# Optimization experiments

Hardware: AMD Instinct MI355X
Metric: run time of the kernel (lower is better)

## Reference

```python
import jax, jax.numpy as jnp
import numpy as np
from jax import lax

WIN = 9  # NCC window per axis (default [9]*3)

# 3x3x3 edge/shape kernels, shape [O=1, I=1, 3, 3, 3]
_LAP = np.zeros((3, 3, 3), np.float32)
_LAP[1, 1, 1] = 6.0
_LAP[0, 1, 1] = _LAP[2, 1, 1] = -1.0
_LAP[1, 0, 1] = _LAP[1, 2, 1] = -1.0
_LAP[1, 1, 0] = _LAP[1, 1, 2] = -1.0
LAP_K = jnp.asarray(_LAP)[None, None]

_row = np.array([[-1.0, 0.0, 1.0], [-2.0, 0.0, 2.0], [-1.0, 0.0, 1.0]], np.float32)
SOBEL_X = jnp.asarray(np.stack([_row, _row, _row], axis=0))[None, None]
_plane = np.array([[-1.0, -2.0, -1.0], [-1.0, -2.0, -1.0], [-1.0, -2.0, -1.0]], np.float32)
SOBEL_Y = jnp.asarray(np.stack([_plane, np.zeros((3, 3), np.float32), -_plane], axis=0))[None, None]
_zp = np.array([[-1.0, -1.0, -1.0], [0.0, 0.0, 0.0], [1.0, 1.0, 1.0]], np.float32)
SOBEL_Z = jnp.asarray(np.stack([_zp, 2.0 * _zp, _zp], axis=0))[None, None]


def conv3d(x, k, pad):
    # x: [N,C,D,H,W], k: [O,I,kd,kh,kw]
    return lax.conv_general_dilated(x, k, (1, 1, 1), [(pad, pad)] * 3)


def box_sum(x, win=WIN):
    # Separable all-ones box filter == dense ones conv (same math, fewer FLOPs)
    pad = win // 2
    for axis in range(3):
        kshape = [1, 1, 1, 1, 1]
        kshape[2 + axis] = win
        k = jnp.ones(kshape, x.dtype)
        padding = [(pad, pad) if a == axis else (0, 0) for a in range(3)]
        x = lax.conv_general_dilated(x, k, (1, 1, 1), padding)
    return x


def ncc_vxm(Ii, Ji, win=WIN):
    win_size = float(win ** 3)
    I2, J2, IJ = Ii * Ii, Ji * Ji, Ii * Ji
    I_sum = box_sum(Ii, win)
    J_sum = box_sum(Ji, win)
    I2_sum = box_sum(I2, win)
    J2_sum = box_sum(J2, win)
    IJ_sum = box_sum(IJ, win)
    u_I = I_sum / win_size
    u_J = J_sum / win_size
    cross = IJ_sum - u_J * I_sum - u_I * J_sum + u_I * u_J * win_size
    I_var = I2_sum - 2.0 * u_I * I_sum + u_I * u_I * win_size
    J_var = J2_sum - 2.0 * u_J * J_sum + u_J * u_J * win_size
    cc = cross * cross / (I_var * J_var + 1e-5)
    return -jnp.mean(cc)


def edge_detection(v):
    return conv3d(v, LAP_K, pad=1)


def shape_detection(v):
    gx = conv3d(v, SOBEL_X, pad=1)
    gy = conv3d(v, SOBEL_Y, pad=1)
    gz = conv3d(v, SOBEL_Z, pad=1)
    return jnp.sqrt(gx * gx + gy * gy + gz * gz)


def setup_inputs() -> dict:
    key = jax.random.key(0)
    k1, k2 = jax.random.split(key)
    shape = (1, 1, 160, 192, 160)
    y_true = jax.random.uniform(k1, shape, dtype=jnp.float32)
    y_pred = jax.random.uniform(k2, shape, dtype=jnp.float32)
    return {"y_true": y_true, "y_pred": y_pred}


def reference(y_true, y_pred):
    loss_orig = ncc_vxm(y_true, y_pred)
    loss_edge = ncc_vxm(edge_detection(y_true), edge_detection(y_pred))
    loss_shape = ncc_vxm(shape_detection(y_true), shape_detection(y_pred))
    return 0.8 * loss_orig + 0.1 * loss_edge + 0.1 * loss_shape
```

## Files before the change

### kernel.cpp

```cpp
#include <hip/hip_runtime.h>
#include <hip/hip_fp16.h>
#include <math.h>

#define DD 160
#define HHH 192
#define WWW 160
constexpr int HW = HHH * WWW;
constexpr int NV = DD * HHH * WWW;
constexpr int W4 = WWW / 4;
constexpr int HC = 4;
constexpr int DC = 4;
constexpr int SC = 8;
constexpr int SCF = 4;

constexpr int NB_WH  = (W4 * DD * (HHH / HC)) / 256;
constexpr int NB_SO  = (W4 * HHH * (DD / SC)) / 256;
constexpr int NB_LAP = (NV / 4) / 256;
constexpr int NB_DCC = (W4 * HHH * (DD / DC)) / 256;
constexpr int NB_FU  = (W4 * HHH * (DD / SCF)) / 256;

__device__ __forceinline__ int xcd_swz(int b, int n) {
    int q = n >> 3;
    return (b & 7) * q + (b >> 3);
}

__device__ __forceinline__ float4 ldg4(const float* __restrict__ p, int idx, bool ok) {
    float4 z = make_float4(0.f, 0.f, 0.f, 0.f);
    return ok ? *(const float4*)(p + idx) : z;
}

__device__ __forceinline__ void st_h4(__half* __restrict__ t, int idx,
                                      float s0, float s1, float s2, float s3) {
    union { __half2 h2[2]; uint2 u; } pk;
    pk.h2[0] = __floats2half2_rn(s0, s1);
    pk.h2[1] = __floats2half2_rn(s2, s3);
    *(uint2*)(t + idx) = pk.u;
}

__device__ __forceinline__ void ld_h4(const __half* __restrict__ t, int idx, float o[4]) {
    union { __half2 h2[2]; uint2 u; } pk;
    pk.u = *(const uint2*)(t + idx);
    o[0] = __low2float(pk.h2[0]); o[1] = __high2float(pk.h2[0]);
    o[2] = __low2float(pk.h2[1]); o[3] = __high2float(pk.h2[1]);
}

__device__ void fused_body(int t, const float* __restrict__ p,
                           __half* __restrict__ olap, __half* __restrict__ osob) {
    int w = (t % W4) * 4;
    int h = (t / W4) % HHH;
    int c = t / (W4 * HHH);
    int d0 = c * SCF;

    float A1[3][4], A2[3][4], A3[3][4];
    float P6[6], PP4[4], PH[4];
#pragma unroll
    for (int j = 0; j < 3; j++)
#pragma unroll
        for (int k = 0; k < 4; k++) { A1[j][k] = 0.f; A2[j][k] = 0.f; A3[j][k] = 0.f; }
#pragma unroll
    for (int k = 0; k < 6; k++) P6[k] = 0.f;
#pragma unroll
    for (int k = 0; k < 4; k++) { PP4[k] = 0.f; PH[k] = 0.f; }

#pragma unroll
    for (int i = 0; i < SCF + 2; i++) {
        int s = d0 - 1 + i;
#pragma unroll
        for (int k = 0; k < 4; k++) {
            A1[0][k] = A1[1][k]; A2[0][k] = A2[1][k]; A3[0][k] = A3[1][k];
            A1[1][k] = A1[2][k]; A2[1][k] = A2[2][k]; A3[1][k] = A3[2][k];
        }
        float C6[6] = {0.f, 0.f, 0.f, 0.f, 0.f, 0.f};
        float CH[4] = {0.f, 0.f, 0.f, 0.f};
#pragma unroll
        for (int k = 0; k < 4; k++) { A1[2][k] = 0.f; A2[2][k] = 0.f; A3[2][k] = 0.f; }
        if (s >= 0 && s < DD) {
#pragma unroll
            for (int kh = -1; kh <= 1; kh++) {
                int h2 = h + kh;
                if ((unsigned)h2 < (unsigned)HHH) {
                    int rb = (s * HHH + h2) * WWW + w;
                    float4 cen = *(const float4*)(p + rb);
                    float xm = (w > 0) ? p[rb - 1] : 0.f;
                    float xp = (w + 4 < WWW) ? p[rb + 4] : 0.f;
                    float xv[6] = {xm, cen.x, cen.y, cen.z, cen.w, xp};
                    float smh = (kh == 0) ? 2.f : 1.f;
                    float grh = (float)kh;
#pragma unroll
                    for (int k = 0; k < 4; k++) {
                        float gw = xv[k + 2] - xv[k];
                        float pw = xv[k] + xv[k + 1] + xv[k + 2];
                        float sw = pw + xv[k + 1];
                        A1[2][k] += smh * gw;
                        A2[2][k] += sw;
                        A3[2][k] += grh * pw;
                    }
                    if (kh == 0) {
#pragma unroll
                        for (int j = 0; j < 6; j++) C6[j] = xv[j];
                    } else {
#pragma unroll
                        for (int k = 0; k < 4; k++) CH[k] += xv[k + 1];
                    }
                }
            }
        }
        if (i >= 2) {
            int d = s - 1;
            int idx = (d * HHH + h) * WWW + w;
            float vs[4], vl[4];
#pragma unroll
            for (int k = 0; k < 4; k++) {
                float gx = A1[0][k] + A1[1][k] + A1[2][k];
                float gy = A2[2][k] - A2[0][k];
                float gz = A3[0][k] + 2.f * A3[1][k] + A3[2][k];
                vs[k] = sqrtf(gx * gx + gy * gy + gz * gz);
                vl[k] = 6.f * P6[k + 1] - (P6[k] + P6[k + 2] + PH[k] + PP4[k] + C6[k + 1]);
            }
            st_h4(osob, idx, vs[0], vs[1], vs[2], vs[3]);
            st_h4(olap, idx, vl[0], vl[1], vl[2], vl[3]);
        }
#pragma unroll
        for (int k = 0; k < 4; k++) PP4[k] = P6[k + 1];
#pragma unroll
        for (int j = 0; j < 6; j++) P6[j] = C6[j];
#pragma unroll
        for (int k = 0; k < 4; k++) PH[k] = CH[k];
    }
}

__device__ __forceinline__ void lap_body(int t, const float* __restrict__ a,
                                         const float* __restrict__ b,
                                         __half* __restrict__ oa, __half* __restrict__ ob) {
    int w = (t % W4) * 4;
    int h = (t / W4) % HHH;
    int d = t / (W4 * HHH);
    int idx = (d * HHH + h) * WWW + w;
    bool dok0 = d > 0, dok1 = d < DD - 1, hok0 = h > 0, hok1 = h < HHH - 1;
#pragma unroll
    for (int s = 0; s < 2; s++) {
        const float* p = s ? b : a;
        __half* o = s ? ob : oa;
        float4 c = *(const float4*)(p + idx);
        float m1 = (w > 0) ? p[idx - 1] : 0.f;
        float p4 = (w + 4 < WWW) ? p[idx + 4] : 0.f;
        float4 dm = ldg4(p, idx - HW, dok0);
        float4 dp = ldg4(p, idx + HW, dok1);
        float4 hm = ldg4(p, idx - WWW, hok0);
        float4 hp = ldg4(p, idx + WWW, hok1);
        st_h4(o, idx,
              6.f * c.x - (m1 + c.y + dm.x + dp.x + hm.x + hp.x),
              6.f * c.y - (c.x + c.z + dm.y + dp.y + hm.y + hp.y),
              6.f * c.z - (c.y + c.w + dm.z + dp.z + hm.z + hp.z),
              6.f * c.w - (c.z + p4 + dm.w + dp.w + hm.w + hp.w));
    }
}

__device__ __forceinline__ void sobel_slice(const float* __restrict__ p, int s, int h, int w,
                                            float a1[4], float a2[4], float a3[4]) {
#pragma unroll
    for (int k = 0; k < 4; k++) { a1[k] = 0.f; a2[k] = 0.f; a3[k] = 0.f; }
#pragma unroll
    for (int kh = -1; kh <= 1; kh++) {
        int h2 = h + kh;
        if ((unsigned)h2 < (unsigned)HHH) {
            int rb = (s * HHH + h2) * WWW + w;
            float4 cen = *(const float4*)(p + rb);
            float xm = (w > 0) ? p[rb - 1] : 0.f;
            float xp = (w + 4 < WWW) ? p[rb + 4] : 0.f;
            float xv[6] = {xm, cen.x, cen.y, cen.z, cen.w, xp};
            float smh = (kh == 0) ? 2.f : 1.f;
            float grh = (float)kh;
#pragma unroll
            for (int k = 0; k < 4; k++) {
                float gw = xv[k + 2] - xv[k];
                float pw = xv[k] + xv[k + 1] + xv[k + 2];
                float sw = pw + xv[k + 1];
                a1[k] += smh * gw;
                a2[k] += sw;
                a3[k] += grh * pw;
            }
        }
    }
}

__device__ __forceinline__ void sobel_body(int t, const float* __restrict__ a,
                                           const float* __restrict__ b,
                                           __half* __restrict__ oa, __half* __restrict__ ob) {
    int w = (t % W4) * 4;
    int h = (t / W4) % HHH;
    int c = t / (W4 * HHH);
    int d0 = c * SC;

    float A1[2][3][4], A2[2][3][4], A3[2][3][4];
#pragma unroll
    for (int r = 0; r < 2; r++)
#pragma unroll
        for (int j = 0; j < 3; j++)
#pragma unroll
            for (int k = 0; k < 4; k++) { A1[r][j][k] = 0.f; A2[r][j][k] = 0.f; A3[r][j][k] = 0.f; }

#pragma unroll
    for (int i = 0; i < SC + 2; i++) {
        int s = d0 - 1 + i;
#pragma unroll
        for (int r = 0; r < 2; r++)
#pragma unroll
            for (int k = 0; k < 4; k++) {
                A1[r][0][k] = A1[r][1][k]; A2[r][0][k] = A2[r][1][k]; A3[r][0][k] = A3[r][1][k];
                A1[r][1][k] = A1[r][2][k]; A2[r][1][k] = A2[r][2][k]; A3[r][1][k] = A3[r][2][k];
            }
        if (s >= 0 && s < DD) {
            sobel_slice(a, s, h, w, A1[0][2], A2[0][2], A3[0][2]);
            sobel_slice(b, s, h, w, A1[1][2], A2[1][2], A3[1][2]);
        } else {
#pragma unroll
            for (int r = 0; r < 2; r++)
#pragma unroll
                for (int k = 0; k < 4; k++) { A1[r][2][k] = 0.f; A2[r][2][k] = 0.f; A3[r][2][k] = 0.f; }
        }
        if (i >= 2) {
            int d = s - 1;
            int idx = (d * HHH + h) * WWW + w;
            float va[4], vb[4];
#pragma unroll
            for (int k = 0; k < 4; k++) {
                float gx = A1[0][0][k] + A1[0][1][k] + A1[0][2][k];
                float gy = A2[0][2][k] - A2[0][0][k];
                float gz = A3[0][0][k] + 2.f * A3[0][1][k] + A3[0][2][k];
                va[k] = sqrtf(gx * gx + gy * gy + gz * gz);
                gx = A1[1][0][k] + A1[1][1][k] + A1[1][2][k];
                gy = A2[1][2][k] - A2[1][0][k];
                gz = A3[1][0][k] + 2.f * A3[1][1][k] + A3[1][2][k];
                vb[k] = sqrtf(gx * gx + gy * gy + gz * gz);
            }
            st_h4(oa, idx, va[0], va[1], va[2], va[3]);
            st_h4(ob, idx, vb[0], vb[1], vb[2], vb[3]);
        }
    }
}

__device__ __forceinline__ void q5_from(const float x[12], const float y[12], float q[5][4]) {
    float s0 = 0, s1 = 0, s2 = 0, s3 = 0, s4 = 0;
#pragma unroll
    for (int j = 0; j < 9; j++) {
        s0 += x[j]; s1 += y[j];
        s2 += x[j] * x[j]; s3 += y[j] * y[j]; s4 += x[j] * y[j];
    }
    q[0][0] = s0; q[1][0] = s1; q[2][0] = s2; q[3][0] = s3; q[4][0] = s4;
#pragma unroll
    for (int k = 1; k < 4; k++) {
        q[0][k] = q[0][k - 1] + x[k + 8] - x[k - 1];
        q[1][k] = q[1][k - 1] + y[k + 8] - y[k - 1];
        q[2][k] = q[2][k - 1] + x[k + 8] * x[k + 8] - x[k - 1] * x[k - 1];
        q[3][k] = q[3][k - 1] + y[k + 8] * y[k + 8] - y[k - 1] * y[k - 1];
        q[4][k] = q[4][k - 1] + x[k + 8] * y[k + 8] - x[k - 1] * y[k - 1];
    }
}

__device__ __forceinline__ void ld12(const float* __restrict__ p, int rowbase, int w, float x[12]) {
    bool lo = (w >= 4);
    bool hi = (w + 7 < WWW);
    float4 x0 = ldg4(p, rowbase + w - 4, lo);
    float4 x1 = *(const float4*)(p + rowbase + w);
    float4 x2 = ldg4(p, rowbase + w + 4, hi);
    x[0] = x0.x; x[1] = x0.y; x[2] = x0.z; x[3] = x0.w;
    x[4] = x1.x; x[5] = x1.y; x[6] = x1.z; x[7] = x1.w;
    x[8] = x2.x; x[9] = x2.y; x[10] = x2.z; x[11] = x2.w;
}

__device__ __forceinline__ void ld12(const __half* __restrict__ p, int rowbase, int w, float x[12]) {
    bool lo = (w >= 4);
    bool hi = (w + 7 < WWW);
    union { __half2 h2[2]; uint2 u; } u0, u1, u2;
    uint2 z = make_uint2(0, 0);
    u0.u = lo ? *(const uint2*)(p + rowbase + w - 4) : z;
    u1.u = *(const uint2*)(p + rowbase + w);
    u2.u = hi ? *(const uint2*)(p + rowbase + w + 4) : z;
    x[0] = __low2float(u0.h2[0]); x[1] = __high2float(u0.h2[0]);
    x[2] = __low2float(u0.h2[1]); x[3] = __high2float(u0.h2[1]);
    x[4] = __low2float(u1.h2[0]); x[5] = __high2float(u1.h2[0]);
    x[6] = __low2float(u1.h2[1]); x[7] = __high2float(u1.h2[1]);
    x[8] = __low2float(u2.h2[0]); x[9] = __high2float(u2.h2[0]);
    x[10] = __low2float(u2.h2[1]); x[11] = __high2float(u2.h2[1]);
}

template <typename T>
__device__ __forceinline__ void rowq5(const T* __restrict__ a, const T* __restrict__ b,
                                      int rowbase, int w, float q[5][4]) {
    float x[12], y[12];
    ld12(a, rowbase, w, x);
    ld12(b, rowbase, w, y);
    q5_from(x, y, q);
}

template <typename T>
__device__ void whsum_body(int t, const T* __restrict__ a, const T* __restrict__ b,
                           __half* __restrict__ t0, __half* __restrict__ t1,
                           __half* __restrict__ t2, __half* __restrict__ t3,
                           __half* __restrict__ t4) {
    int w = (t % W4) * 4;
    int d = (t / W4) % DD;
    int c = t / (W4 * DD);
    int h0 = c * HC;

    float S[5][4] = {{0}};
    for (int j = 0; j < 9; j++) {
        int r = h0 - 4 + j;
        if ((unsigned)r < (unsigned)HHH) {
            float q[5][4];
            rowq5(a, b, (d * HHH + r) * WWW, w, q);
#pragma unroll
            for (int qq = 0; qq < 5; qq++)
#pragma unroll
                for (int k = 0; k < 4; k++) S[qq][k] += q[qq][k];
        }
    }
    {
        int idx = (d * HHH + h0) * WWW + w;
        st_h4(t0, idx, S[0][0], S[0][1], S[0][2], S[0][3]);
        st_h4(t1, idx, S[1][0], S[1][1], S[1][2], S[1][3]);
        st_h4(t2, idx, S[2][0], S[2][1], S[2][2], S[2][3]);
        st_h4(t3, idx, S[3][0], S[3][1], S[3][2], S[3][3]);
        st_h4(t4, idx, S[4][0], S[4][1], S[4][2], S[4][3]);
    }
    for (int h = h0 + 1; h < h0 + HC; h++) {
        int rin = h + 4, rout = h - 5;
        if (rin < HHH) {
            float q[5][4];
            rowq5(a, b, (d * HHH + rin) * WWW, w, q);
#pragma unroll
            for (int qq = 0; qq < 5; qq++)
#pragma unroll
                for (int k = 0; k < 4; k++) S[qq][k] += q[qq][k];
        }
        if (rout >= 0) {
            float q[5][4];
            rowq5(a, b, (d * HHH + rout) * WWW, w, q);
#pragma unroll
            for (int qq = 0; qq < 5; qq++)
#pragma unroll
                for (int k = 0; k < 4; k++) S[qq][k] -= q[qq][k];
        }
        int idx = (d * HHH + h) * WWW + w;
        st_h4(t0, idx, S[0][0], S[0][1], S[0][2], S[0][3]);
        st_h4(t1, idx, S[1][0], S[1][1], S[1][2], S[1][3]);
        st_h4(t2, idx, S[2][0], S[2][1], S[2][2], S[2][3]);
        st_h4(t3, idx, S[3][0], S[3][1], S[3][2], S[3][3]);
        st_h4(t4, idx, S[4][0], S[4][1], S[4][2], S[4][3]);
    }
}

__device__ __forceinline__ float cc1(float s0, float s1, float s2, float s3, float s4) {
    const float wsz = 729.0f;
    const float inv = 1.0f / 729.0f;
    float uI = s0 * inv;
    float uJ = s1 * inv;
    float cross = s4 - uJ * s0 - uI * s1 + uI * uJ * wsz;
    float Iv = s2 - 2.0f * uI * s0 + uI * uI * wsz;
    float Jv = s3 - 2.0f * uJ * s1 + uJ * uJ * wsz;
    return cross * cross / (Iv * Jv + 1e-5f);
}

__device__ void dcc_body(int t, const __half* __restrict__ t0, const __half* __restrict__ t1,
                         const __half* __restrict__ t2, const __half* __restrict__ t3,
                         const __half* __restrict__ t4, double* __restrict__ acc, int pair) {
    int w = (t % W4) * 4;
    int h = (t / W4) % HHH;
    int c = t / (W4 * HHH);
    int d0 = c * DC;

    float S[5][4] = {{0}};
    for (int j = 0; j < 9; j++) {
        int r = d0 - 4 + j;
        if ((unsigned)r < (unsigned)DD) {
            int idx = (r * HHH + h) * WWW + w;
            float v[5][4];
            ld_h4(t0, idx, v[0]); ld_h4(t1, idx, v[1]); ld_h4(t2, idx, v[2]);
            ld_h4(t3, idx, v[3]); ld_h4(t4, idx, v[4]);
#pragma unroll
            for (int q = 0; q < 5; q++)
#pragma unroll
                for (int k = 0; k < 4; k++) S[q][k] += v[q][k];
        }
    }
    float local = 0.f;
#pragma unroll
    for (int k = 0; k < 4; k++) local += cc1(S[0][k], S[1][k], S[2][k], S[3][k], S[4][k]);
#pragma unroll
    for (int d = 1; d < DC; d++) {
        int rin = d0 + d + 4, rout = d0 + d - 5;
        if (rin < DD) {
            int idx = (rin * HHH + h) * WWW + w;
            float v[5][4];
            ld_h4(t0, idx, v[0]); ld_h4(t1, idx, v[1]); ld_h4(t2, idx, v[2]);
            ld_h4(t3, idx, v[3]); ld_h4(t4, idx, v[4]);
#pragma unroll
            for (int q = 0; q < 5; q++)
#pragma unroll
                for (int k = 0; k < 4; k++) S[q][k] += v[q][k];
        }
        if (rout >= 0) {
            int idx = (rout * HHH + h) * WWW + w;
            float v[5][4];
            ld_h4(t0, idx, v[0]); ld_h4(t1, idx, v[1]); ld_h4(t2, idx, v[2]);
            ld_h4(t3, idx, v[3]); ld_h4(t4, idx, v[4]);
#pragma unroll
            for (int q = 0; q < 5; q++)
#pragma unroll
                for (int k = 0; k < 4; k++) S[q][k] -= v[q][k];
        }
#pragma unroll
        for (int k = 0; k < 4; k++) local += cc1(S[0][k], S[1][k], S[2][k], S[3][k], S[4][k]);
    }

    for (int off = 32; off > 0; off >>= 1) local += __shfl_down(local, off);
    __shared__ float wsum_[4];
    if ((threadIdx.x & 63) == 0) wsum_[threadIdx.x >> 6] = local;
    __syncthreads();
    if (threadIdx.x == 0) {
        float s = wsum_[0] + wsum_[1] + wsum_[2] + wsum_[3];
        atomicAdd(&acc[pair], (double)s);
    }
}

__global__ void __launch_bounds__(256, 4)
stage1f(const float* __restrict__ yt, const float* __restrict__ yp,
        __half* __restrict__ e1a, __half* __restrict__ e1b,
        __half* __restrict__ e2a, __half* __restrict__ e2b,
        double* __restrict__ acc) {
    int b = blockIdx.x;
    if (b < NB_FU) {
        int lb = xcd_swz(b, NB_FU);
        fused_body(lb * 256 + threadIdx.x, yt, e1a, e2a);
    } else if (b < 2 * NB_FU) {
        int lb = xcd_swz(b - NB_FU, NB_FU);
        fused_body(lb * 256 + threadIdx.x, yp, e1b, e2b);
    } else {
        if (threadIdx.x < 3) acc[threadIdx.x] = 0.0;
    }
}

__global__ void stage2w(const float* __restrict__ yt, const float* __restrict__ yp,
                        const __half* __restrict__ e1a, const __half* __restrict__ e1b,
                        const __half* __restrict__ e2a, const __half* __restrict__ e2b,
                        __half* __restrict__ tA, __half* __restrict__ tB,
                        __half* __restrict__ tC) {
    int b = blockIdx.x;
    size_t nv = (size_t)NV;
    if (b < NB_WH) {
        int lb = xcd_swz(b, NB_WH);
        whsum_body<float>(lb * 256 + threadIdx.x, yt, yp,
                          tA, tA + nv, tA + 2 * nv, tA + 3 * nv, tA + 4 * nv);
    } else if (b < 2 * NB_WH) {
        int lb = xcd_swz(b - NB_WH, NB_WH);
        whsum_body<__half>(lb * 256 + threadIdx.x, e1a, e1b,
                           tB, tB + nv, tB + 2 * nv, tB + 3 * nv, tB + 4 * nv);
    } else {
        int lb = xcd_swz(b - 2 * NB_WH, NB_WH);
        whsum_body<__half>(lb * 256 + threadIdx.x, e2a, e2b,
                           tC, tC + nv, tC + 2 * nv, tC + 3 * nv, tC + 4 * nv);
    }
}

__global__ void stage3w(const __half* __restrict__ tA, const __half* __restrict__ tB,
                        const __half* __restrict__ tC, double* __restrict__ acc) {
    int b = blockIdx.x;
    size_t nv = (size_t)NV;
    if (b < NB_DCC) {
        int lb = xcd_swz(b, NB_DCC);
        dcc_body(lb * 256 + threadIdx.x,
                 tA, tA + nv, tA + 2 * nv, tA + 3 * nv, tA + 4 * nv, acc, 0);
    } else if (b < 2 * NB_DCC) {
        int lb = xcd_swz(b - NB_DCC, NB_DCC);
        dcc_body(lb * 256 + threadIdx.x,
                 tB, tB + nv, tB + 2 * nv, tB + 3 * nv, tB + 4 * nv, acc, 1);
    } else {
        int lb = xcd_swz(b - 2 * NB_DCC, NB_DCC);
        dcc_body(lb * 256 + threadIdx.x,
                 tC, tC + nv, tC + 2 * nv, tC + 3 * nv, tC + 4 * nv, acc, 2);
    }
}

__global__ void stage1(const float* __restrict__ yt, const float* __restrict__ yp,
                       __half* __restrict__ e1a, __half* __restrict__ e1b,
                       __half* __restrict__ e2a, __half* __restrict__ e2b,
                       __half* __restrict__ ta0, __half* __restrict__ ta1,
                       __half* __restrict__ ta2, __half* __restrict__ ta3,
                       __half* __restrict__ ta4, double* __restrict__ acc) {
    int b = blockIdx.x;
    if (b < NB_WH) {
        int lb = xcd_swz(b, NB_WH);
        whsum_body<float>(lb * 256 + threadIdx.x, yt, yp, ta0, ta1, ta2, ta3, ta4);
    } else if (b < NB_WH + NB_SO) {
        int lb = xcd_swz(b - NB_WH, NB_SO);
        sobel_body(lb * 256 + threadIdx.x, yt, yp, e2a, e2b);
    } else if (b < NB_WH + NB_SO + NB_LAP) {
        int lb = xcd_swz(b - NB_WH - NB_SO, NB_LAP);
        lap_body(lb * 256 + threadIdx.x, yt, yp, e1a, e1b);
    } else {
        if (threadIdx.x < 3) acc[threadIdx.x] = 0.0;
    }
}

__global__ void stage23(const __half* __restrict__ ea, const __half* __restrict__ eb,
                        __half* __restrict__ o0, __half* __restrict__ o1,
                        __half* __restrict__ o2, __half* __restrict__ o3,
                        __half* __restrict__ o4,
                        const __half* __restrict__ i0, const __half* __restrict__ i1,
                        const __half* __restrict__ i2, const __half* __restrict__ i3,
                        const __half* __restrict__ i4, double* __restrict__ acc, int pair) {
    int b = blockIdx.x;
    if (b < NB_WH) {
        int lb = xcd_swz(b, NB_WH);
        whsum_body<__half>(lb * 256 + threadIdx.x, ea, eb, o0, o1, o2, o3, o4);
    } else {
        int lb = xcd_swz(b - NB_WH, NB_DCC);
        dcc_body(lb * 256 + threadIdx.x, i0, i1, i2, i3, i4, acc, pair);
    }
}

__global__ void dcc_k(const __half* __restrict__ t0, const __half* __restrict__ t1,
                      const __half* __restrict__ t2, const __half* __restrict__ t3,
                      const __half* __restrict__ t4, double* __restrict__ acc, int pair) {
    int lb = xcd_swz(blockIdx.x, NB_DCC);
    dcc_body(lb * 256 + threadIdx.x, t0, t1, t2, t3, t4, acc, pair);
}

__global__ void finalize_k(const double* __restrict__ acc, float* __restrict__ out) {
    if (threadIdx.x == 0) {
        double v = 0.8 * acc[0] + 0.1 * acc[1] + 0.1 * acc[2];
        out[0] = (float)(-v / (double)NV);
    }
}

extern "C" void kernel_launch(void* const* d_in, const int* in_sizes, int n_in,
                              void* d_out, int out_size, void* d_ws, size_t ws_size,
                              hipStream_t stream) {
    const float* yt = (const float*)d_in[0];
    const float* yp = (const float*)d_in[1];
    float* out = (float*)d_out;

    double* acc = (double*)d_ws;
    __half* base = (__half*)((char*)d_ws + 256);
    size_t nv = (size_t)NV;
    __half* e1a = base + 0 * nv;
    __half* e1b = base + 1 * nv;
    __half* e2a = base + 2 * nv;
    __half* e2b = base + 3 * nv;
    __half* tA = base + 4 * nv;
    __half* tB = base + 9 * nv;
    __half* tC = base + 14 * nv;

    bool wide = ws_size >= 256 + 19 * nv * sizeof(__half);

    dim3 blk(256);

    if (wide) {
        hipLaunchKernelGGL(stage1f, dim3(2 * NB_FU + 1), blk, 0, stream,
                           yt, yp, e1a, e1b, e2a, e2b, acc);
        hipLaunchKernelGGL(stage2w, dim3(3 * NB_WH), blk, 0, stream,
                           yt, yp, e1a, e1b, e2a, e2b, tA, tB, tC);
        hipLaunchKernelGGL(stage3w, dim3(3 * NB_DCC), blk, 0, stream,
                           tA, tB, tC, acc);
    } else {
        hipLaunchKernelGGL(stage1, dim3(NB_WH + NB_SO + NB_LAP + 1), blk, 0, stream,
                           yt, yp, e1a, e1b, e2a, e2b,
                           tA, tA + nv, tA + 2 * nv, tA + 3 * nv, tA + 4 * nv, acc);
        hipLaunchKernelGGL(stage23, dim3(NB_WH + NB_DCC), blk, 0, stream,
                           e1a, e1b,
                           tB, tB + nv, tB + 2 * nv, tB + 3 * nv, tB + 4 * nv,
                           tA, tA + nv, tA + 2 * nv, tA + 3 * nv, tA + 4 * nv,
                           acc, 0);
        hipLaunchKernelGGL(stage23, dim3(NB_WH + NB_DCC), blk, 0, stream,
                           e2a, e2b,
                           tA, tA + nv, tA + 2 * nv, tA + 3 * nv, tA + 4 * nv,
                           tB, tB + nv, tB + 2 * nv, tB + 3 * nv, tB + 4 * nv,
                           acc, 1);
        hipLaunchKernelGGL(dcc_k, dim3(NB_DCC), blk, 0, stream,
                           tA, tA + nv, tA + 2 * nv, tA + 3 * nv, tA + 4 * nv, acc, 2);
    }

    hipLaunchKernelGGL(finalize_k, dim3(1), dim3(1), 0, stream, acc, out);
}
```

Baseline: 344.9 us.

## Interleave five box-sum planes per 4-wide group and rebalance stage work

```diff
diff --git a/kernel.cpp b/kernel.cpp
--- a/kernel.cpp
+++ b/kernel.cpp
@@ -37,11 +37,26 @@
     *(uint2*)(t + idx) = pk.u;
 }
 
-__device__ __forceinline__ void ld_h4(const __half* __restrict__ t, int idx, float o[4]) {
-    union { __half2 h2[2]; uint2 u; } pk;
-    pk.u = *(const uint2*)(t + idx);
-    o[0] = __low2float(pk.h2[0]); o[1] = __high2float(pk.h2[0]);
-    o[2] = __low2float(pk.h2[1]); o[3] = __high2float(pk.h2[1]);
+__device__ __forceinline__ void st_t5(__half* __restrict__ t, int g, const float S[5][4]) {
+    __half* p = t + (size_t)g * 20;
+#pragma unroll
+    for (int q = 0; q < 5; q++) {
+        union { __half2 h2[2]; uint2 u; } pk;
+        pk.h2[0] = __floats2half2_rn(S[q][0], S[q][1]);
+        pk.h2[1] = __floats2half2_rn(S[q][2], S[q][3]);
+        *(uint2*)(p + q * 4) = pk.u;
+    }
+}
+
+__device__ __forceinline__ void ld_t5(const __half* __restrict__ t, int g, float v[5][4]) {
+    const __half* p = t + (size_t)g * 20;
+#pragma unroll
+    for (int q = 0; q < 5; q++) {
+        union { __half2 h2[2]; uint2 u; } pk;
+        pk.u = *(const uint2*)(p + q * 4);
+        v[q][0] = __low2float(pk.h2[0]); v[q][1] = __high2float(pk.h2[0]);
+        v[q][2] = __low2float(pk.h2[1]); v[q][3] = __high2float(pk.h2[1]);
+    }
 }
 
 __device__ void fused_body(int t, const float* __restrict__ p,
@@ -295,13 +310,12 @@
 }
 
 template <typename T>
-__device__ void whsum_body(int t, const T* __restrict__ a, const T* __restrict__ b,
-                           __half* __restrict__ t0, __half* __restrict__ t1,
-                           __half* __restrict__ t2, __half* __restrict__ t3,
-                           __half* __restrict__ t4) {
-    int w = (t % W4) * 4;
-    int d = (t / W4) % DD;
-    int c = t / (W4 * DD);
+__device__ void whsum_body(int t_, const T* __restrict__ a, const T* __restrict__ b,
+                           __half* __restrict__ t) {
+    int w4 = t_ % W4;
+    int w = w4 * 4;
+    int d = (t_ / W4) % DD;
+    int c = t_ / (W4 * DD);
     int h0 = c * HC;
 
     float S[5][4] = {{0}};
@@ -316,14 +330,7 @@
                 for (int k = 0; k < 4; k++) S[qq][k] += q[qq][k];
         }
     }
-    {
-        int idx = (d * HHH + h0) * WWW + w;
-        st_h4(t0, idx, S[0][0], S[0][1], S[0][2], S[0][3]);
-        st_h4(t1, idx, S[1][0], S[1][1], S[1][2], S[1][3]);
-        st_h4(t2, idx, S[2][0], S[2][1], S[2][2], S[2][3]);
-        st_h4(t3, idx, S[3][0], S[3][1], S[3][2], S[3][3]);
-        st_h4(t4, idx, S[4][0], S[4][1], S[4][2], S[4][3]);
-    }
+    st_t5(t, (d * HHH + h0) * W4 + w4, S);
     for (int h = h0 + 1; h < h0 + HC; h++) {
         int rin = h + 4, rout = h - 5;
         if (rin < HHH) {
@@ -342,12 +349,7 @@
 #pragma unroll
                 for (int k = 0; k < 4; k++) S[qq][k] -= q[qq][k];
         }
-        int idx = (d * HHH + h) * WWW + w;
-        st_h4(t0, idx, S[0][0], S[0][1], S[0][2], S[0][3]);
-        st_h4(t1, idx, S[1][0], S[1][1], S[1][2], S[1][3]);
-        st_h4(t2, idx, S[2][0], S[2][1], S[2][2], S[2][3]);
-        st_h4(t3, idx, S[3][0], S[3][1], S[3][2], S[3][3]);
-        st_h4(t4, idx, S[4][0], S[4][1], S[4][2], S[4][3]);
+        st_t5(t, (d * HHH + h) * W4 + w4, S);
     }
 }
 
@@ -362,22 +364,19 @@
     return cross * cross / (Iv * Jv + 1e-5f);
 }
 
-__device__ void dcc_body(int t, const __half* __restrict__ t0, const __half* __restrict__ t1,
-                         const __half* __restrict__ t2, const __half* __restrict__ t3,
-                         const __half* __restrict__ t4, double* __restrict__ acc, int pair) {
-    int w = (t % W4) * 4;
-    int h = (t / W4) % HHH;
-    int c = t / (W4 * HHH);
+__device__ void dcc_body(int t_, const __half* __restrict__ tile,
+                         double* __restrict__ acc, int pair) {
+    int w4 = t_ % W4;
+    int h = (t_ / W4) % HHH;
+    int c = t_ / (W4 * HHH);
     int d0 = c * DC;
 
     float S[5][4] = {{0}};
     for (int j = 0; j < 9; j++) {
         int r = d0 - 4 + j;
         if ((unsigned)r < (unsigned)DD) {
-            int idx = (r * HHH + h) * WWW + w;
             float v[5][4];
-            ld_h4(t0, idx, v[0]); ld_h4(t1, idx, v[1]); ld_h4(t2, idx, v[2]);
-            ld_h4(t3, idx, v[3]); ld_h4(t4, idx, v[4]);
+            ld_t5(tile, (r * HHH + h) * W4 + w4, v);
 #pragma unroll
             for (int q = 0; q < 5; q++)
 #pragma unroll
@@ -391,20 +390,16 @@
     for (int d = 1; d < DC; d++) {
         int rin = d0 + d + 4, rout = d0 + d - 5;
         if (rin < DD) {
-            int idx = (rin * HHH + h) * WWW + w;
             float v[5][4];
-            ld_h4(t0, idx, v[0]); ld_h4(t1, idx, v[1]); ld_h4(t2, idx, v[2]);
-            ld_h4(t3, idx, v[3]); ld_h4(t4, idx, v[4]);
+            ld_t5(tile, (rin * HHH + h) * W4 + w4, v);
 #pragma unroll
             for (int q = 0; q < 5; q++)
 #pragma unroll
                 for (int k = 0; k < 4; k++) S[q][k] += v[q][k];
         }
         if (rout >= 0) {
-            int idx = (rout * HHH + h) * WWW + w;
             float v[5][4];
-            ld_h4(t0, idx, v[0]); ld_h4(t1, idx, v[1]); ld_h4(t2, idx, v[2]);
-            ld_h4(t3, idx, v[3]); ld_h4(t4, idx, v[4]);
+            ld_t5(tile, (rout * HHH + h) * W4 + w4, v);
 #pragma unroll
             for (int q = 0; q < 5; q++)
 #pragma unroll
@@ -425,10 +420,10 @@
 }
 
 __global__ void __launch_bounds__(256, 4)
-stage1f(const float* __restrict__ yt, const float* __restrict__ yp,
+stage1w(const float* __restrict__ yt, const float* __restrict__ yp,
         __half* __restrict__ e1a, __half* __restrict__ e1b,
         __half* __restrict__ e2a, __half* __restrict__ e2b,
-        double* __restrict__ acc) {
+        __half* __restrict__ tA, double* __restrict__ acc) {
     int b = blockIdx.x;
     if (b < NB_FU) {
         int lb = xcd_swz(b, NB_FU);
@@ -436,62 +431,51 @@
     } else if (b < 2 * NB_FU) {
         int lb = xcd_swz(b - NB_FU, NB_FU);
         fused_body(lb * 256 + threadIdx.x, yp, e1b, e2b);
+    } else if (b < 2 * NB_FU + NB_WH) {
+        int lb = xcd_swz(b - 2 * NB_FU, NB_WH);
+        whsum_body<float>(lb * 256 + threadIdx.x, yt, yp, tA);
     } else {
         if (threadIdx.x < 3) acc[threadIdx.x] = 0.0;
     }
 }
 
-__global__ void stage2w(const float* __restrict__ yt, const float* __restrict__ yp,
-                        const __half* __restrict__ e1a, const __half* __restrict__ e1b,
+__global__ void stage2m(const __half* __restrict__ e1a, const __half* __restrict__ e1b,
                         const __half* __restrict__ e2a, const __half* __restrict__ e2b,
-                        __half* __restrict__ tA, __half* __restrict__ tB,
-                        __half* __restrict__ tC) {
+                        __half* __restrict__ tB, __half* __restrict__ tC,
+                        const __half* __restrict__ tA, double* __restrict__ acc) {
     int b = blockIdx.x;
-    size_t nv = (size_t)NV;
     if (b < NB_WH) {
         int lb = xcd_swz(b, NB_WH);
-        whsum_body<float>(lb * 256 + threadIdx.x, yt, yp,
-                          tA, tA + nv, tA + 2 * nv, tA + 3 * nv, tA + 4 * nv);
+        whsum_body<__half>(lb * 256 + threadIdx.x, e1a, e1b, tB);
     } else if (b < 2 * NB_WH) {
         int lb = xcd_swz(b - NB_WH, NB_WH);
-        whsum_body<__half>(lb * 256 + threadIdx.x, e1a, e1b,
-                           tB, tB + nv, tB + 2 * nv, tB + 3 * nv, tB + 4 * nv);
+        whsum_body<__half>(lb * 256 + threadIdx.x, e2a, e2b, tC);
     } else {
-        int lb = xcd_swz(b - 2 * NB_WH, NB_WH);
-        whsum_body<__half>(lb * 256 + threadIdx.x, e2a, e2b,
-                           tC, tC + nv, tC + 2 * nv, tC + 3 * nv, tC + 4 * nv);
-    }
-}
-
-__global__ void stage3w(const __half* __restrict__ tA, const __half* __restrict__ tB,
-                        const __half* __restrict__ tC, double* __restrict__ acc) {
+        int lb = xcd_swz(b - 2 * NB_WH, NB_DCC);
+        dcc_body(lb * 256 + threadIdx.x, tA, acc, 0);
+    }
+}
+
+__global__ void stage3m(const __half* __restrict__ tB, const __half* __restrict__ tC,
+                        double* __restrict__ acc) {
     int b = blockIdx.x;
-    size_t nv = (size_t)NV;
     if (b < NB_DCC) {
         int lb = xcd_swz(b, NB_DCC);
-        dcc_body(lb * 256 + threadIdx.x,
-                 tA, tA + nv, tA + 2 * nv, tA + 3 * nv, tA + 4 * nv, acc, 0);
-    } else if (b < 2 * NB_DCC) {
+        dcc_body(lb * 256 + threadIdx.x, tB, acc, 1);
+    } else {
         int lb = xcd_swz(b - NB_DCC, NB_DCC);
-        dcc_body(lb * 256 + threadIdx.x,
-                 tB, tB + nv, tB + 2 * nv, tB + 3 * nv, tB + 4 * nv, acc, 1);
-    } else {
-        int lb = xcd_swz(b - 2 * NB_DCC, NB_DCC);
-        dcc_body(lb * 256 + threadIdx.x,
-                 tC, tC + nv, tC + 2 * nv, tC + 3 * nv, tC + 4 * nv, acc, 2);
+        dcc_body(lb * 256 + threadIdx.x, tC, acc, 2);
     }
 }
 
 __global__ void stage1(const float* __restrict__ yt, const float* __restrict__ yp,
                        __half* __restrict__ e1a, __half* __restrict__ e1b,
                        __half* __restrict__ e2a, __half* __restrict__ e2b,
-                       __half* __restrict__ ta0, __half* __restrict__ ta1,
-                       __half* __restrict__ ta2, __half* __restrict__ ta3,
-                       __half* __restrict__ ta4, double* __restrict__ acc) {
+                       __half* __restrict__ tA, double* __restrict__ acc) {
     int b = blockIdx.x;
     if (b < NB_WH) {
         int lb = xcd_swz(b, NB_WH);
-        whsum_body<float>(lb * 256 + threadIdx.x, yt, yp, ta0, ta1, ta2, ta3, ta4);
+        whsum_body<float>(lb * 256 + threadIdx.x, yt, yp, tA);
     } else if (b < NB_WH + NB_SO) {
         int lb = xcd_swz(b - NB_WH, NB_SO);
         sobel_body(lb * 256 + threadIdx.x, yt, yp, e2a, e2b);
@@ -504,27 +488,21 @@
 }
 
 __global__ void stage23(const __half* __restrict__ ea, const __half* __restrict__ eb,
-                        __half* __restrict__ o0, __half* __restrict__ o1,
-                        __half* __restrict__ o2, __half* __restrict__ o3,
-                        __half* __restrict__ o4,
-                        const __half* __restrict__ i0, const __half* __restrict__ i1,
-                        const __half* __restrict__ i2, const __half* __restrict__ i3,
-                        const __half* __restrict__ i4, double* __restrict__ acc, int pair) {
+                        __half* __restrict__ o, const __half* __restrict__ i,
+                        double* __restrict__ acc, int pair) {
     int b = blockIdx.x;
     if (b < NB_WH) {
         int lb = xcd_swz(b, NB_WH);
-        whsum_body<__half>(lb * 256 + threadIdx.x, ea, eb, o0, o1, o2, o3, o4);
+        whsum_body<__half>(lb * 256 + threadIdx.x, ea, eb, o);
     } else {
         int lb = xcd_swz(b - NB_WH, NB_DCC);
-        dcc_body(lb * 256 + threadIdx.x, i0, i1, i2, i3, i4, acc, pair);
-    }
-}
-
-__global__ void dcc_k(const __half* __restrict__ t0, const __half* __restrict__ t1,
-                      const __half* __restrict__ t2, const __half* __restrict__ t3,
-                      const __half* __restrict__ t4, double* __restrict__ acc, int pair) {
+        dcc_body(lb * 256 + threadIdx.x, i, acc, pair);
+    }
+}
+
+__global__ void dcc_k(const __half* __restrict__ tile, double* __restrict__ acc, int pair) {
     int lb = xcd_swz(blockIdx.x, NB_DCC);
-    dcc_body(lb * 256 + threadIdx.x, t0, t1, t2, t3, t4, acc, pair);
+    dcc_body(lb * 256 + threadIdx.x, tile, acc, pair);
 }
 
 __global__ void finalize_k(const double* __restrict__ acc, float* __restrict__ out) {
@@ -557,28 +535,19 @@
     dim3 blk(256);
 
     if (wide) {
-        hipLaunchKernelGGL(stage1f, dim3(2 * NB_FU + 1), blk, 0, stream,
-                           yt, yp, e1a, e1b, e2a, e2b, acc);
-        hipLaunchKernelGGL(stage2w, dim3(3 * NB_WH), blk, 0, stream,
-                           yt, yp, e1a, e1b, e2a, e2b, tA, tB, tC);
-        hipLaunchKernelGGL(stage3w, dim3(3 * NB_DCC), blk, 0, stream,
-                           tA, tB, tC, acc);
+        hipLaunchKernelGGL(stage1w, dim3(2 * NB_FU + NB_WH + 1), blk, 0, stream,
+                           yt, yp, e1a, e1b, e2a, e2b, tA, acc);
+        hipLaunchKernelGGL(stage2m, dim3(2 * NB_WH + NB_DCC), blk, 0, stream,
+                           e1a, e1b, e2a, e2b, tB, tC, tA, acc);
+        hipLaunchKernelGGL(stage3m, dim3(2 * NB_DCC), blk, 0, stream, tB, tC, acc);
     } else {
         hipLaunchKernelGGL(stage1, dim3(NB_WH + NB_SO + NB_LAP + 1), blk, 0, stream,
-                           yt, yp, e1a, e1b, e2a, e2b,
-                           tA, tA + nv, tA + 2 * nv, tA + 3 * nv, tA + 4 * nv, acc);
+                           yt, yp, e1a, e1b, e2a, e2b, tA, acc);
         hipLaunchKernelGGL(stage23, dim3(NB_WH + NB_DCC), blk, 0, stream,
-                           e1a, e1b,
-                           tB, tB + nv, tB + 2 * nv, tB + 3 * nv, tB + 4 * nv,
-                           tA, tA + nv, tA + 2 * nv, tA + 3 * nv, tA + 4 * nv,
-                           acc, 0);
+                           e1a, e1b, tB, tA, acc, 0);
         hipLaunchKernelGGL(stage23, dim3(NB_WH + NB_DCC), blk, 0, stream,
-                           e2a, e2b,
-                           tA, tA + nv, tA + 2 * nv, tA + 3 * nv, tA + 4 * nv,
-                           tB, tB + nv, tB + 2 * nv, tB + 3 * nv, tB + 4 * nv,
-                           acc, 1);
-        hipLaunchKernelGGL(dcc_k, dim3(NB_DCC), blk, 0, stream,
-                           tA, tA + nv, tA + 2 * nv, tA + 3 * nv, tA + 4 * nv, acc, 2);
+                           e2a, e2b, tA, tB, acc, 1);
+        hipLaunchKernelGGL(dcc_k, dim3(NB_DCC), blk, 0, stream, tA, acc, 2);
     }
 
     hipLaunchKernelGGL(finalize_k, dim3(1), dim3(1), 0, stream, acc, out);
```

After: 334.3 us, median of 2. 1.03x faster.
